# Performance work log

Measured on AMD Instinct MI355X. Metric: run time of the kernel, lower is better.

## Reference

```python
import jax, jax.numpy as jnp
import numpy as np

N_CHILDS = 50000
N_EDGES = 500000
NODE_FEAT = 256
NUM_SEM = 57
HID = 256
EDGE_FEAT = 64
EDGE_TYPES = 4
NUM_ITERS = 2


def setup_inputs() -> dict:
    key = jax.random.key(0)
    ks = jax.random.split(key, 12)
    d_in = NODE_FEAT + NUM_SEM            # 313
    d_ne = 2 * HID + EDGE_FEAT + EDGE_TYPES  # 580
    d_par = HID * (NUM_ITERS + 1)         # 768
    def lin(k, fan_in, fan_out):
        kw, kb = jax.random.split(k)
        s = 1.0 / np.sqrt(fan_in)
        return (jax.random.uniform(kw, (fan_in, fan_out), jnp.float32, -s, s),
                jax.random.uniform(kb, (fan_out,), jnp.float32, -s, s))
    W_child, b_child = lin(ks[0], d_in, HID)
    W_ne0, b_ne0 = lin(ks[1], d_ne, HID)
    W_ne1, b_ne1 = lin(ks[2], d_ne, HID)
    W_parent, b_parent = lin(ks[3], d_par, NODE_FEAT)
    return {
        "child_feats": jax.random.normal(ks[4], (1, N_CHILDS, d_in), jnp.float32),
        "child_exists": jnp.ones((1, N_CHILDS, 1), jnp.float32),
        "edge_type_onehot": jax.random.normal(ks[5], (1, N_EDGES, EDGE_TYPES), jnp.float32),
        "edge_feats": jax.random.normal(ks[6], (1, N_EDGES, EDGE_FEAT), jnp.float32),
        "edge_indices": jax.random.randint(ks[7], (1, N_EDGES, 2), 0, N_CHILDS, jnp.int64),
        "W_child": W_child, "b_child": b_child,
        "W_ne0": W_ne0, "b_ne0": b_ne0,
        "W_ne1": W_ne1, "b_ne1": b_ne1,
        "W_parent": W_parent, "b_parent": b_parent,
    }


def reference(child_feats, child_exists, edge_type_onehot, edge_feats, edge_indices,
              W_child, b_child, W_ne0, b_ne0, W_ne1, b_ne1, W_parent, b_parent):
    n = child_feats.shape[1]
    # node embedding: linear + relu, mask non-existent children
    x = jax.nn.relu(jnp.einsum('bnd,dh->bnh', child_feats, W_child) + b_child)
    x = x * child_exists                              # [1, N, H]
    iter_parent = [x.max(axis=1)]                     # symmetric_type == 'max'
    ef = jnp.concatenate([edge_type_onehot, edge_feats], axis=2)[0]  # [E, 4+64]
    src = edge_indices[0, :, 0]
    dst = edge_indices[0, :, 1]
    cnt = jax.ops.segment_sum(jnp.ones((src.shape[0],), x.dtype), src, num_segments=n)
    denom = jnp.maximum(cnt, 1.0)[:, None]            # scatter_mean clamp
    for W, b in ((W_ne0, b_ne0), (W_ne1, b_ne1)):
        nef = jnp.concatenate([x[0, src], x[0, dst], ef], axis=1)  # [E, 580]
        nef = jax.nn.relu(nef @ W + b)                # [E, H]
        # edge_symmetric_type == 'avg': scatter_mean over source index
        x = (jax.ops.segment_sum(nef, src, num_segments=n) / denom)[None]
        iter_parent.append(x.max(axis=1))
    parent = jnp.concatenate(iter_parent, axis=1)     # [1, H*(iters+1)]
    return jax.nn.relu(parent @ W_parent + b_parent)  # [1, node_feat_size]
```

## Files before the change

### kernel.cpp

```cpp
#include <hip/hip_runtime.h>

#define NC   50000
#define NE   500000
#define NEP  (NE + 64)
#define DIN  313
#define DNE  580
#define KPC  320
#define KB   96
#define NB_SCAN 196

typedef __attribute__((ext_vector_type(8))) short bf16x8;
typedef __attribute__((ext_vector_type(4))) float f32x4;

static __device__ __forceinline__ unsigned short f2bf(float f) {
    unsigned u = __float_as_uint(f);
    unsigned r = (u + 0x7fff + ((u >> 16) & 1)) >> 16;
    return (unsigned short)r;
}
static __device__ __forceinline__ float bf2f(unsigned short u) {
    return __uint_as_float(((unsigned)u) << 16);
}
static __device__ __forceinline__ void gload_lds16(const unsigned short* g, unsigned short* l) {
    __builtin_amdgcn_global_load_lds(
        (const __attribute__((address_space(1))) unsigned int*)(g),
        (__attribute__((address_space(3))) unsigned int*)(l), 16, 0, 0);
}

__global__ __launch_bounds__(256) void prep_w_kernel(
    const float* __restrict__ W0, const float* __restrict__ W1,
    const float* __restrict__ Wc,
    unsigned short* __restrict__ Wpt, unsigned short* __restrict__ Wbt,
    unsigned short* __restrict__ Wct)
{
    int b = blockIdx.x;
    if (b < 1024) {
        int layer = b >> 9, n2 = b & 511;
        const float* W = layer ? W1 : W0;
        unsigned short* dst = Wpt + (size_t)layer * 512 * 256 + (size_t)n2 * 256;
        int t = threadIdx.x;
        int ch = t >> 5, s = (t >> 3) & 3, j = t & 7;
        int gk = ch * 32 + ((s ^ (n2 & 3)) * 8) + j;
        float v = (n2 < 256) ? W[(size_t)gk * 256 + n2] : W[(size_t)(256 + gk) * 256 + (n2 - 256)];
        dst[t] = f2bf(v);
    } else if (b < 1536) {
        int idx = b - 1024;
        int layer = idx >> 8, n = idx & 255;
        const float* W = layer ? W1 : W0;
        unsigned short* dst = Wbt + (size_t)layer * 256 * KB + (size_t)n * KB;
        int t = threadIdx.x;
        if (t < KB) {
            int ch = t >> 5, s = (t >> 3) & 3, j = t & 7;
            int gk = ch * 32 + ((s ^ (n & 3)) * 8) + j;
            float v = (512 + gk < DNE) ? W[(size_t)(512 + gk) * 256 + n] : 0.0f;
            dst[t] = f2bf(v);
        }
    } else {
        int n = b - 1536;
        unsigned short* dst = Wct + (size_t)n * KPC;
        for (int t = threadIdx.x; t < KPC; t += 256) {
            int ch = t >> 5, s = (t >> 3) & 3, j = t & 7;
            int gk = ch * 32 + ((s ^ (n & 3)) * 8) + j;
            float v = (gk < DIN) ? Wc[(size_t)gk * 256 + n] : 0.0f;
            dst[t] = f2bf(v);
        }
    }
}

__global__ __launch_bounds__(256, 4) void child_mfma_kernel(
    const float* __restrict__ cf, const float* __restrict__ exists,
    const unsigned short* __restrict__ Wct, const float* __restrict__ bias,
    unsigned short* __restrict__ xb, float* __restrict__ pmax)
{
    __shared__ unsigned short sA[64][40];
    __shared__ unsigned short sB[256][32];
    __shared__ float smax[256];

    const int tid = threadIdx.x, lane = tid & 63, wid = tid >> 6;
    const int wm = wid >> 1, wn = wid & 1, l15 = lane & 15, l4 = lane >> 4;
    const int node0 = blockIdx.x * 64;
    const int arow = tid >> 2, s3 = tid & 3;

    smax[tid] = 0.0f;

    f32x4 acc[2][8];
    #pragma unroll
    for (int mi = 0; mi < 2; ++mi)
        #pragma unroll
        for (int ni = 0; ni < 8; ++ni)
            acc[mi][ni] = (f32x4){0.f, 0.f, 0.f, 0.f};

    int nodeA = node0 + arow; if (nodeA >= NC) nodeA = NC - 1;

    for (int ch = 0; ch < 10; ++ch) {
        #pragma unroll
        for (int i = 0; i < 4; ++i) {
            int n = (wid << 6) + (i << 4) + (lane >> 2);
            gload_lds16(Wct + (size_t)n * KPC + ch * 32 + (lane & 3) * 8,
                        &sB[(wid << 6) + (i << 4)][0]);
        }
        {
            int gk0 = ch * 32 + s3 * 8;
            union { unsigned short u[8]; int4 v; } pk;
            #pragma unroll
            for (int j = 0; j < 8; ++j) {
                int gk = gk0 + j;
                float f = (gk < DIN) ? cf[(size_t)nodeA * DIN + gk] : 0.0f;
                pk.u[j] = f2bf(f);
            }
            *(int4*)&sA[arow][s3 * 8] = pk.v;
        }
        __syncthreads();
        bf16x8 af[2];
        #pragma unroll
        for (int mi = 0; mi < 2; ++mi)
            af[mi] = *(const bf16x8*)&sA[wm * 32 + mi * 16 + l15][l4 * 8];
        #pragma unroll
        for (int ni = 0; ni < 8; ++ni) {
            int n = wn * 128 + ni * 16 + l15;
            bf16x8 bfr = *(const bf16x8*)&sB[n][(l4 ^ (n & 3)) * 8];
            acc[0][ni] = __builtin_amdgcn_mfma_f32_16x16x32_bf16(af[0], bfr, acc[0][ni], 0, 0, 0);
            acc[1][ni] = __builtin_amdgcn_mfma_f32_16x16x32_bf16(af[1], bfr, acc[1][ni], 0, 0, 0);
        }
        __syncthreads();
    }

    float bv[8];
    #pragma unroll
    for (int ni = 0; ni < 8; ++ni) bv[ni] = bias[wn * 128 + ni * 16 + l15];
    float cmax[8];
    #pragma unroll
    for (int ni = 0; ni < 8; ++ni) cmax[ni] = 0.0f;

    #pragma unroll
    for (int mi = 0; mi < 2; ++mi) {
        #pragma unroll
        for (int r = 0; r < 4; ++r) {
            int node = node0 + wm * 32 + mi * 16 + l4 * 4 + r;
            if (node < NC) {
                float ex = exists[node];
                #pragma unroll
                for (int ni = 0; ni < 8; ++ni) {
                    float v = fmaxf(acc[mi][ni][r] + bv[ni], 0.f) * ex;
                    xb[(size_t)node * 256 + wn * 128 + ni * 16 + l15] = f2bf(v);
                    cmax[ni] = fmaxf(cmax[ni], v);
                }
            }
        }
    }
    #pragma unroll
    for (int ni = 0; ni < 8; ++ni)
        atomicMax((unsigned int*)&smax[wn * 128 + ni * 16 + l15], __float_as_uint(cmax[ni]));
    __syncthreads();
    atomicMax((unsigned int*)&pmax[tid], __float_as_uint(smax[tid]));
}

__global__ __launch_bounds__(256, 3) void node_gemm_kernel(
    const unsigned short* __restrict__ xb,
    const unsigned short* __restrict__ Wpt,
    unsigned short* __restrict__ yp)
{
    __shared__ unsigned short sA[2][64][40];
    __shared__ unsigned short sB[2][256][32];

    const int tid = threadIdx.x, lane = tid & 63, wid = tid >> 6;
    const int wm = wid >> 1, wn = wid & 1, l15 = lane & 15, l4 = lane >> 4;
    const int node0 = blockIdx.x * 64;
    const int n0 = blockIdx.y * 256;
    const int arow = tid >> 2, s3 = tid & 3;

    int nodeA = node0 + arow; if (nodeA >= NC) nodeA = NC - 1;

    f32x4 acc[2][8];
    #pragma unroll
    for (int mi = 0; mi < 2; ++mi)
        #pragma unroll
        for (int ni = 0; ni < 8; ++ni)
            acc[mi][ni] = (f32x4){0.f, 0.f, 0.f, 0.f};

    #pragma unroll
    for (int i = 0; i < 4; ++i) {
        int n = (wid << 6) + (i << 4) + (lane >> 2);
        gload_lds16(Wpt + (size_t)(n0 + n) * 256 + (lane & 3) * 8, &sB[0][(wid << 6) + (i << 4)][0]);
    }
    *(int4*)&sA[0][arow][s3 * 8] = *(const int4*)(xb + (size_t)nodeA * 256 + s3 * 8);
    __syncthreads();

    int buf = 0;
    for (int ch = 0; ch < 8; ++ch) {
        const int nch = ch + 1;
        int4 areg;
        if (nch < 8) {
            #pragma unroll
            for (int i = 0; i < 4; ++i) {
                int n = (wid << 6) + (i << 4) + (lane >> 2);
                gload_lds16(Wpt + (size_t)(n0 + n) * 256 + nch * 32 + (lane & 3) * 8,
                            &sB[buf ^ 1][(wid << 6) + (i << 4)][0]);
            }
            areg = *(const int4*)(xb + (size_t)nodeA * 256 + nch * 32 + s3 * 8);
        }
        bf16x8 af[2];
        #pragma unroll
        for (int mi = 0; mi < 2; ++mi)
            af[mi] = *(const bf16x8*)&sA[buf][wm * 32 + mi * 16 + l15][l4 * 8];
        #pragma unroll
        for (int ni = 0; ni < 8; ++ni) {
            int n = wn * 128 + ni * 16 + l15;
            bf16x8 bfr = *(const bf16x8*)&sB[buf][n][(l4 ^ (n & 3)) * 8];
            acc[0][ni] = __builtin_amdgcn_mfma_f32_16x16x32_bf16(af[0], bfr, acc[0][ni], 0, 0, 0);
            acc[1][ni] = __builtin_amdgcn_mfma_f32_16x16x32_bf16(af[1], bfr, acc[1][ni], 0, 0, 0);
        }
        if (nch < 8) *(int4*)&sA[buf ^ 1][arow][s3 * 8] = areg;
        __syncthreads();
        buf ^= 1;
    }

    #pragma unroll
    for (int mi = 0; mi < 2; ++mi) {
        #pragma unroll
        for (int r = 0; r < 4; ++r) {
            int node = node0 + wm * 32 + mi * 16 + l4 * 4 + r;
            if (node < NC) {
                #pragma unroll
                for (int ni = 0; ni < 8; ++ni)
                    yp[(size_t)node * 512 + n0 + wn * 128 + ni * 16 + l15] = f2bf(acc[mi][ni][r]);
            }
        }
    }
}

__global__ __launch_bounds__(256, 3) void node_gemm_scaled_kernel(
    const float* __restrict__ accb, const float* __restrict__ invv,
    const unsigned short* __restrict__ Wpt,
    unsigned short* __restrict__ yp, float* __restrict__ pmax0)
{
    __shared__ unsigned short sA[2][64][40];
    __shared__ unsigned short sB[2][256][32];
    __shared__ float smax[256];

    const int tid = threadIdx.x, lane = tid & 63, wid = tid >> 6;
    const int wm = wid >> 1, wn = wid & 1, l15 = lane & 15, l4 = lane >> 4;
    const int node0 = blockIdx.x * 64;
    const int n0 = blockIdx.y * 256;
    const int arow = tid >> 2, s3 = tid & 3;

    smax[tid] = 0.0f;

    int nodeA = node0 + arow; if (nodeA >= NC) nodeA = NC - 1;
    const float inv_n = invv[nodeA];

    f32x4 acc[2][8];
    #pragma unroll
    for (int mi = 0; mi < 2; ++mi)
        #pragma unroll
        for (int ni = 0; ni < 8; ++ni)
            acc[mi][ni] = (f32x4){0.f, 0.f, 0.f, 0.f};

    #pragma unroll
    for (int i = 0; i < 4; ++i) {
        int n = (wid << 6) + (i << 4) + (lane >> 2);
        gload_lds16(Wpt + (size_t)(n0 + n) * 256 + (lane & 3) * 8, &sB[0][(wid << 6) + (i << 4)][0]);
    }
    {
        float4 a0 = *(const float4*)(accb + (size_t)nodeA * 256 + s3 * 8);
        float4 a1 = *(const float4*)(accb + (size_t)nodeA * 256 + s3 * 8 + 4);
        float v0=a0.x*inv_n, v1=a0.y*inv_n, v2=a0.z*inv_n, v3=a0.w*inv_n;
        float v4=a1.x*inv_n, v5=a1.y*inv_n, v6=a1.z*inv_n, v7=a1.w*inv_n;
        union { unsigned short u[8]; int4 v; } pk;
        pk.u[0]=f2bf(v0); pk.u[1]=f2bf(v1); pk.u[2]=f2bf(v2); pk.u[3]=f2bf(v3);
        pk.u[4]=f2bf(v4); pk.u[5]=f2bf(v5); pk.u[6]=f2bf(v6); pk.u[7]=f2bf(v7);
        *(int4*)&sA[0][arow][s3 * 8] = pk.v;
        int c0 = s3 * 8;
        atomicMax((unsigned int*)&smax[c0+0], __float_as_uint(v0));
        atomicMax((unsigned int*)&smax[c0+1], __float_as_uint(v1));
        atomicMax((unsigned int*)&smax[c0+2], __float_as_uint(v2));
        atomicMax((unsigned int*)&smax[c0+3], __float_as_uint(v3));
        atomicMax((unsigned int*)&smax[c0+4], __float_as_uint(v4));
        atomicMax((unsigned int*)&smax[c0+5], __float_as_uint(v5));
        atomicMax((unsigned int*)&smax[c0+6], __float_as_uint(v6));
        atomicMax((unsigned int*)&smax[c0+7], __float_as_uint(v7));
    }
    __syncthreads();

    int buf = 0;
    for (int ch = 0; ch < 8; ++ch) {
        const int nch = ch + 1;
        float4 f4a, f4b;
        if (nch < 8) {
            #pragma unroll
            for (int i = 0; i < 4; ++i) {
                int n = (wid << 6) + (i << 4) + (lane >> 2);
                gload_lds16(Wpt + (size_t)(n0 + n) * 256 + nch * 32 + (lane & 3) * 8,
                            &sB[buf ^ 1][(wid << 6) + (i << 4)][0]);
            }
            f4a = *(const float4*)(accb + (size_t)nodeA * 256 + nch * 32 + s3 * 8);
            f4b = *(const float4*)(accb + (size_t)nodeA * 256 + nch * 32 + s3 * 8 + 4);
        }
        bf16x8 af[2];
        #pragma unroll
        for (int mi = 0; mi < 2; ++mi)
            af[mi] = *(const bf16x8*)&sA[buf][wm * 32 + mi * 16 + l15][l4 * 8];
        #pragma unroll
        for (int ni = 0; ni < 8; ++ni) {
            int n = wn * 128 + ni * 16 + l15;
            bf16x8 bfr = *(const bf16x8*)&sB[buf][n][(l4 ^ (n & 3)) * 8];
            acc[0][ni] = __builtin_amdgcn_mfma_f32_16x16x32_bf16(af[0], bfr, acc[0][ni], 0, 0, 0);
            acc[1][ni] = __builtin_amdgcn_mfma_f32_16x16x32_bf16(af[1], bfr, acc[1][ni], 0, 0, 0);
        }
        if (nch < 8) {
            float v0=f4a.x*inv_n, v1=f4a.y*inv_n, v2=f4a.z*inv_n, v3=f4a.w*inv_n;
            float v4=f4b.x*inv_n, v5=f4b.y*inv_n, v6=f4b.z*inv_n, v7=f4b.w*inv_n;
            union { unsigned short u[8]; int4 v; } pk;
            pk.u[0]=f2bf(v0); pk.u[1]=f2bf(v1); pk.u[2]=f2bf(v2); pk.u[3]=f2bf(v3);
            pk.u[4]=f2bf(v4); pk.u[5]=f2bf(v5); pk.u[6]=f2bf(v6); pk.u[7]=f2bf(v7);
            *(int4*)&sA[buf ^ 1][arow][s3 * 8] = pk.v;
            int c0 = nch * 32 + s3 * 8;
            atomicMax((unsigned int*)&smax[c0+0], __float_as_uint(v0));
            atomicMax((unsigned int*)&smax[c0+1], __float_as_uint(v1));
            atomicMax((unsigned int*)&smax[c0+2], __float_as_uint(v2));
            atomicMax((unsigned int*)&smax[c0+3], __float_as_uint(v3));
            atomicMax((unsigned int*)&smax[c0+4], __float_as_uint(v4));
            atomicMax((unsigned int*)&smax[c0+5], __float_as_uint(v5));
            atomicMax((unsigned int*)&smax[c0+6], __float_as_uint(v6));
            atomicMax((unsigned int*)&smax[c0+7], __float_as_uint(v7));
        }
        __syncthreads();
        buf ^= 1;
    }

    #pragma unroll
    for (int mi = 0; mi < 2; ++mi) {
        #pragma unroll
        for (int r = 0; r < 4; ++r) {
            int node = node0 + wm * 32 + mi * 16 + l4 * 4 + r;
            if (node < NC) {
                #pragma unroll
                for (int ni = 0; ni < 8; ++ni)
                    yp[(size_t)node * 512 + n0 + wn * 128 + ni * 16 + l15] = f2bf(acc[mi][ni][r]);
            }
        }
    }
    atomicMax((unsigned int*)&pmax0[tid], __float_as_uint(smax[tid]));
}

__global__ __launch_bounds__(256) void count_int_kernel(
    const int* __restrict__ eidx, int* __restrict__ icnt)
{
    int t = blockIdx.x * 256 + threadIdx.x;
    if (t < NE) atomicAdd(&icnt[eidx[2 * t]], 1);
}

__global__ __launch_bounds__(256) void scan1_kernel(
    const int* __restrict__ icnt, int* __restrict__ part)
{
    __shared__ int sd[256];
    int i = blockIdx.x * 256 + threadIdx.x;
    sd[threadIdx.x] = (i < NC) ? icnt[i] : 0;
    __syncthreads();
    for (int d = 128; d > 0; d >>= 1) {
        if (threadIdx.x < d) sd[threadIdx.x] += sd[threadIdx.x + d];
        __syncthreads();
    }
    if (threadIdx.x == 0) part[blockIdx.x] = sd[0];
}

__global__ void scan2_kernel(int* __restrict__ part)
{
    if (threadIdx.x == 0) {
        int acc = 0;
        for (int i = 0; i < NB_SCAN; ++i) { int v = part[i]; part[i] = acc; acc += v; }
    }
}

__global__ __launch_bounds__(256) void scan3_kernel(
    const int* __restrict__ icnt, const int* __restrict__ part,
    int* __restrict__ cur)
{
    __shared__ int sc[256];
    const int t = threadIdx.x;
    int i = blockIdx.x * 256 + t;
    int val = (i < NC) ? icnt[i] : 0;
    sc[t] = val;
    __syncthreads();
    for (int d = 1; d < 256; d <<= 1) {
        int x = (t >= d) ? sc[t - d] : 0;
        __syncthreads();
        sc[t] += x;
        __syncthreads();
    }
    if (i < NC) cur[i] = part[blockIdx.x] + sc[t] - val;
}

__global__ __launch_bounds__(256) void bin_kernel(
    const int* __restrict__ eidx, int* __restrict__ cur, int* __restrict__ perm)
{
    int t = blockIdx.x * 256 + threadIdx.x;
    if (t < NE) {
        int s = eidx[2 * t];
        int p = atomicAdd(&cur[s], 1);
        perm[p] = t;
    }
}

__global__ __launch_bounds__(256) void inv_kernel(
    const int* __restrict__ icnt, float* __restrict__ inv)
{
    int t = blockIdx.x * 256 + threadIdx.x;
    if (t < NC) inv[t] = 1.0f / fmaxf((float)icnt[t], 1.0f);
}

__global__ __launch_bounds__(256) void ef_prep_kernel(
    const float* __restrict__ eto, const float* __restrict__ efe,
    const int* __restrict__ perm, const int* __restrict__ eidx,
    unsigned short* __restrict__ efc01, unsigned short* __restrict__ efc2,
    int* __restrict__ esrc, int* __restrict__ edst)
{
    int p = blockIdx.x * 256 + threadIdx.x;
    if (p >= NE) return;
    int e = perm[p];
    esrc[p] = eidx[2 * e];
    edst[p] = eidx[2 * e + 1];
    const float* efr = efe + (size_t)e * 64;

    union { unsigned short u[8]; int4 v; } pk;
    {
        float4 a = *(const float4*)(eto + (size_t)e * 4);
        float4 b = *(const float4*)(efr + 0);
        pk.u[0]=f2bf(a.x); pk.u[1]=f2bf(a.y); pk.u[2]=f2bf(a.z); pk.u[3]=f2bf(a.w);
        pk.u[4]=f2bf(b.x); pk.u[5]=f2bf(b.y); pk.u[6]=f2bf(b.z); pk.u[7]=f2bf(b.w);
        *(int4*)(efc01 + (size_t)p * 32) = pk.v;
    }
    #pragma unroll
    for (int g = 1; g < 4; ++g) {
        float4 a = *(const float4*)(efr + g * 8 - 4);
        float4 b = *(const float4*)(efr + g * 8);
        pk.u[0]=f2bf(a.x); pk.u[1]=f2bf(a.y); pk.u[2]=f2bf(a.z); pk.u[3]=f2bf(a.w);
        pk.u[4]=f2bf(b.x); pk.u[5]=f2bf(b.y); pk.u[6]=f2bf(b.z); pk.u[7]=f2bf(b.w);
        *(int4*)(efc01 + (size_t)p * 32 + g * 8) = pk.v;
    }
    #pragma unroll
    for (int g = 0; g < 4; ++g) {
        float4 a = *(const float4*)(efr + 28 + g * 8);
        float4 b = *(const float4*)(efr + 32 + g * 8);
        pk.u[0]=f2bf(a.x); pk.u[1]=f2bf(a.y); pk.u[2]=f2bf(a.z); pk.u[3]=f2bf(a.w);
        pk.u[4]=f2bf(b.x); pk.u[5]=f2bf(b.y); pk.u[6]=f2bf(b.z); pk.u[7]=f2bf(b.w);
        *(int4*)(efc01 + ((size_t)NEP + p) * 32 + g * 8) = pk.v;
    }
    {
        float4 a = *(const float4*)(efr + 60);
        pk.u[0]=f2bf(a.x); pk.u[1]=f2bf(a.y); pk.u[2]=f2bf(a.z); pk.u[3]=f2bf(a.w);
        pk.u[4]=0; pk.u[5]=0; pk.u[6]=0; pk.u[7]=0;
        *(int4*)(efc2 + (size_t)p * 8) = pk.v;
    }
}

#define LOAD16(B, YT, YM)                                              \
    _Pragma("unroll")                                                  \
    for (int r = 0; r < 16; ++r) {                                     \
        int row = (B) * 16 + r;                                        \
        YT[r] = bf2f(yp[((unsigned)s_src[row] << 9) + (unsigned)col]); \
        YM[r] = bf2f(yp[((unsigned)s_dst[row] << 9) + 256u + (unsigned)col]); \
    }

#define WALK16(B, YT, YM)                                              \
    _Pragma("unroll")                                                  \
    for (int r = 0; r < 16; ++r) {                                     \
        int row = (B) * 16 + r;                                        \
        float v = 0.0f;                                                \
        if (e0 + row < NE)                                             \
            v = fmaxf(bf2f(epb[row][col]) + YT[r] + YM[r] + b_col, 0.f); \
        int sr = s_src[row];                                           \
        if (sr != curn) {                                              \
            if (rstart > 0) accb[(size_t)curn * 256 + col] = run;      \
            else            atomicAdd(&accb[(size_t)curn * 256 + col], run); \
            curn = sr; run = v; rstart = row;                          \
        } else {                                                       \
            run += v;                                                  \
        }                                                              \
    }

__global__ __launch_bounds__(256, 4) void combine_efc_kernel(
    const unsigned short* __restrict__ yp,
    const unsigned short* __restrict__ efc01,
    const unsigned short* __restrict__ efc2,
    const int* __restrict__ esrc, const int* __restrict__ edst,
    const unsigned short* __restrict__ Wbt,
    const float* __restrict__ bias,
    float* __restrict__ accb)
{
    __shared__ __align__(16) unsigned char smem[34816];
    unsigned short (*sA01)[64][32] = (unsigned short (*)[64][32])(smem);
    unsigned short (*sA2)[8]       = (unsigned short (*)[8])(smem + 8192);
    unsigned short (*sW)[32]       = (unsigned short (*)[32])(smem + 9216);
    unsigned short (*epb)[272]     = (unsigned short (*)[272])(smem);
    __shared__ int s_src[64], s_dst[64];

    const int tid = threadIdx.x;
    const int nwg = gridDim.x;
    const int q = nwg >> 3, rr = nwg & 7;
    const int xcd = blockIdx.x & 7, within = blockIdx.x >> 3;
    const int bid = (xcd < rr ? xcd * (q + 1) : rr * (q + 1) + (xcd - rr) * q) + within;
    const int e0 = bid * 64;

    const int lane = tid & 63;
    const int wid  = tid >> 6;
    const int wm   = wid >> 1;
    const int wn   = wid & 1;
    const int l15  = lane & 15;
    const int l4   = lane >> 4;

    if (tid < 64) {
        int e = e0 + tid; if (e > NE - 1) e = NE - 1;
        s_src[tid] = esrc[e];
        s_dst[tid] = edst[e];
    }
    gload_lds16(efc01 + ((size_t)e0 + wid * 16) * 32 + lane * 8, &sA01[0][wid * 16][0]);
    gload_lds16(efc01 + ((size_t)NEP + e0 + wid * 16) * 32 + lane * 8, &sA01[1][wid * 16][0]);
    if (wid == 0)
        gload_lds16(efc2 + (size_t)e0 * 8 + lane * 8, &sA2[0][0]);
    #pragma unroll
    for (int i = 0; i < 4; ++i) {
        gload_lds16(Wbt + (size_t)((wid << 6) + (i << 4) + (lane >> 2)) * KB + (lane & 3) * 8,
                    &sW[(wid << 6) + (i << 4)][0]);
    }
    __syncthreads();

    f32x4 acc[2][8];
    #pragma unroll
    for (int mi = 0; mi < 2; ++mi)
        #pragma unroll
        for (int ni = 0; ni < 8; ++ni)
            acc[mi][ni] = (f32x4){0.f, 0.f, 0.f, 0.f};

    #pragma unroll
    for (int ch = 0; ch < 3; ++ch) {
        if (ch > 0) {
            __syncthreads();
            #pragma unroll
            for (int i = 0; i < 4; ++i) {
                gload_lds16(Wbt + (size_t)((wid << 6) + (i << 4) + (lane >> 2)) * KB + ch * 32 + (lane & 3) * 8,
                            &sW[(wid << 6) + (i << 4)][0]);
            }
            __syncthreads();
        }
        bf16x8 af0, af1;
        if (ch < 2) {
            af0 = *(const bf16x8*)&sA01[ch][wm * 32 + l15][l4 * 8];
            af1 = *(const bf16x8*)&sA01[ch][wm * 32 + 16 + l15][l4 * 8];
        } else {
            bf16x8 z = (bf16x8){0,0,0,0,0,0,0,0};
            bf16x8 a0 = *(const bf16x8*)&sA2[wm * 32 + l15][0];
            bf16x8 a1 = *(const bf16x8*)&sA2[wm * 32 + 16 + l15][0];
            af0 = (l4 == 0) ? a0 : z;
            af1 = (l4 == 0) ? a1 : z;
        }
        #pragma unroll
        for (int ni = 0; ni < 8; ++ni) {
            int n = wn * 128 + ni * 16 + l15;
            bf16x8 bfr = *(const bf16x8*)&sW[n][(l4 ^ (n & 3)) * 8];
            acc[0][ni] = __builtin_amdgcn_mfma_f32_16x16x32_bf16(af0, bfr, acc[0][ni], 0, 0, 0);
            acc[1][ni] = __builtin_amdgcn_mfma_f32_16x16x32_bf16(af1, bfr, acc[1][ni], 0, 0, 0);
        }
    }
    __syncthreads();

    #pragma unroll
    for (int mi = 0; mi < 2; ++mi)
        #pragma unroll
        for (int ni = 0; ni < 8; ++ni)
            #pragma unroll
            for (int r = 0; r < 4; ++r)
                epb[wm * 32 + mi * 16 + l4 * 4 + r][wn * 128 + ni * 16 + l15] = f2bf(acc[mi][ni][r]);

    const int col = tid;
    const float b_col = bias[col];
    float ytA[16], ymA[16], ytB[16], ymB[16];
    LOAD16(0, ytA, ymA)
    LOAD16(1, ytB, ymB)
    __syncthreads();

    int curn = s_src[0];
    int rstart = 0;
    float run = 0.f;

    WALK16(0, ytA, ymA)
    LOAD16(2, ytA, ymA)
    WALK16(1, ytB, ymB)
    LOAD16(3, ytB, ymB)
    WALK16(2, ytA, ymA)
    WALK16(3, ytB, ymB)

    atomicAdd(&accb[(size_t)curn * 256 + col], run);
}

__global__ __launch_bounds__(256, 3) void combine_f32_kernel(
    const unsigned short* __restrict__ yp,
    const float* __restrict__ eto, const float* __restrict__ efe,
    const int* __restrict__ eidx, const int* __restrict__ perm,
    const unsigned short* __restrict__ Wbt,
    const float* __restrict__ bias,
    float* __restrict__ accb)
{
    __shared__ unsigned short sA[3][64][40];
    __shared__ unsigned short sW[2][256][32];
    __shared__ int s_src[64], s_dst[64], s_perm[64];

    const int tid = threadIdx.x;
    const int nwg = gridDim.x;
    const int q = nwg >> 3, rr = nwg & 7;
    const int xcd = blockIdx.x & 7, within = blockIdx.x >> 3;
    const int bid = (xcd < rr ? xcd * (q + 1) : rr * (q + 1) + (xcd - rr) * q) + within;
    const int e0 = bid * 64;

    if (tid < 64) {
        int ee = e0 + tid; if (ee >= NE) ee = NE - 1;
        int e = perm[ee];
        s_perm[tid] = e;
        s_src[tid] = eidx[2 * e];
        s_dst[tid] = eidx[2 * e + 1];
    }
    const int lane = tid & 63;
    const int wid  = tid >> 6;
    const int wm   = wid >> 1;
    const int wn   = wid & 1;
    const int l15  = lane & 15;
    const int l4   = lane >> 4;
    const int arow = tid >> 2;
    const int s3   = tid & 3;

    f32x4 acc[2][8];
    #pragma unroll
    for (int mi = 0; mi < 2; ++mi)
        #pragma unroll
        for (int ni = 0; ni < 8; ++ni)
            acc[mi][ni] = (f32x4){0.f, 0.f, 0.f, 0.f};

    #pragma unroll
    for (int i = 0; i < 4; ++i) {
        int n = (wid << 6) + (i << 4) + (lane >> 2);
        gload_lds16(Wbt + (size_t)n * KB + (lane & 3) * 8, &sW[0][(wid << 6) + (i << 4)][0]);
    }
    __syncthreads();

    const int my_e = s_perm[arow];
    #pragma unroll
    for (int ch = 0; ch < 3; ++ch) {
        int g0 = ch * 32 + s3 * 8;
        union { unsigned short u[8]; int4 v; } pk;
        #pragma unroll
        for (int j = 0; j < 8; ++j) {
            int g = g0 + j;
            float f = 0.0f;
            if (g < 4)       f = eto[(size_t)my_e * 4 + g];
            else if (g < 68) f = efe[(size_t)my_e * 64 + (g - 4)];
            pk.u[j] = f2bf(f);
        }
        *(int4*)&sA[ch][arow][s3 * 8] = pk.v;
    }
    __syncthreads();

    int buf = 0;
    #pragma unroll
    for (int ch = 0; ch < 3; ++ch) {
        if (ch + 1 < 3) {
            #pragma unroll
            for (int i = 0; i < 4; ++i) {
                int n = (wid << 6) + (i << 4) + (lane >> 2);
                gload_lds16(Wbt + (size_t)n * KB + (ch + 1) * 32 + (lane & 3) * 8,
                            &sW[buf ^ 1][(wid << 6) + (i << 4)][0]);
            }
        }
        bf16x8 af[2];
        #pragma unroll
        for (int mi = 0; mi < 2; ++mi)
            af[mi] = *(const bf16x8*)&sA[ch][wm * 32 + mi * 16 + l15][l4 * 8];
        #pragma unroll
        for (int ni = 0; ni < 8; ++ni) {
            int n = wn * 128 + ni * 16 + l15;
            bf16x8 bfr = *(const bf16x8*)&sW[buf][n][(l4 ^ (n & 3)) * 8];
            acc[0][ni] = __builtin_amdgcn_mfma_f32_16x16x32_bf16(af[0], bfr, acc[0][ni], 0, 0, 0);
            acc[1][ni] = __builtin_amdgcn_mfma_f32_16x16x32_bf16(af[1], bfr, acc[1][ni], 0, 0, 0);
        }
        __syncthreads();
        buf ^= 1;
    }

    float (*ep)[258] = (float (*)[258])(&sW[0][0][0]);
    const int col = tid;
    const float b_col = bias[col];

    int curn = s_src[0];
    int rstart = 0;
    float run = 0.f;
    #pragma unroll
    for (int c = 0; c < 4; ++c) {
        if (wm == (c >> 1)) {
            const int mi = c & 1;
            #pragma unroll
            for (int ni = 0; ni < 8; ++ni) {
                #pragma unroll
                for (int r = 0; r < 4; ++r)
                    ep[l4 * 4 + r][wn * 128 + ni * 16 + l15] = acc[mi][ni][r];
            }
        }
        float yt[16], ym[16];
        #pragma unroll
        for (int r = 0; r < 16; ++r) {
            int row = c * 16 + r;
            yt[r] = bf2f(yp[(size_t)s_src[row] * 512 + col]);
            ym[r] = bf2f(yp[(size_t)s_dst[row] * 512 + 256 + col]);
        }
        __syncthreads();
        #pragma unroll
        for (int r = 0; r < 16; ++r) {
            int row = c * 16 + r;
            float v = 0.0f;
            if (e0 + row < NE)
                v = fmaxf(ep[r][col] + yt[r] + ym[r] + b_col, 0.f);
            int sr = s_src[row];
            if (sr != curn) {
                if (rstart > 0) accb[(size_t)curn * 256 + col] = run;
                else            atomicAdd(&accb[(size_t)curn * 256 + col], run);
                curn = sr; run = v; rstart = row;
            } else {
                run += v;
            }
        }
        __syncthreads();
    }
    atomicAdd(&accb[(size_t)curn * 256 + col], run);
}

__global__ __launch_bounds__(256) void finalize_kernel(
    const float* __restrict__ src, const float* __restrict__ inv,
    unsigned short* __restrict__ xb_out, float* __restrict__ pmax, int n)
{
    const int tid = threadIdx.x;
    int i0 = blockIdx.x * 128;
    int iend = i0 + 128; if (iend > n) iend = n;
    float m = 0.0f;
    for (int i = i0; i < iend; ++i) {
        float v = src[(size_t)i * 256 + tid];
        v *= inv[i];
        xb_out[(size_t)i * 256 + tid] = f2bf(v);
        m = fmaxf(m, v);
    }
    atomicMax((unsigned int*)&pmax[tid], __float_as_uint(m));
}

__global__ __launch_bounds__(256) void pmax_only_kernel(
    const float* __restrict__ src, const float* __restrict__ inv,
    float* __restrict__ pmax, int n)
{
    const int tid = threadIdx.x;
    int i0 = blockIdx.x * 128;
    int iend = i0 + 128; if (iend > n) iend = n;
    float m = 0.0f;
    for (int i = i0; i < iend; ++i)
        m = fmaxf(m, src[(size_t)i * 256 + tid] * inv[i]);
    atomicMax((unsigned int*)&pmax[tid], __float_as_uint(m));
}

__global__ __launch_bounds__(256) void parent_kernel(
    const float* __restrict__ pmax, const float* __restrict__ W,
    const float* __restrict__ bias, float* __restrict__ out)
{
    __shared__ float sp[768];
    const int tid = threadIdx.x;
    for (int i = tid; i < 768; i += 256) sp[i] = pmax[i];
    __syncthreads();
    float s = bias[tid];
    for (int k = 0; k < 768; ++k) s = fmaf(sp[k], W[(size_t)k * 256 + tid], s);
    out[tid] = fmaxf(s, 0.f);
}

extern "C" void kernel_launch(void* const* d_in, const int* in_sizes, int n_in,
                              void* d_out, int out_size, void* d_ws, size_t ws_size,
                              hipStream_t stream)
{
    const float* cf   = (const float*)d_in[0];
    const float* ex   = (const float*)d_in[1];
    const float* eto  = (const float*)d_in[2];
    const float* efe  = (const float*)d_in[3];
    const int*   eidx = (const int*)d_in[4];
    const float* Wc   = (const float*)d_in[5];
    const float* bc   = (const float*)d_in[6];
    const float* W0   = (const float*)d_in[7];
    const float* b0   = (const float*)d_in[8];
    const float* W1   = (const float*)d_in[9];
    const float* b1   = (const float*)d_in[10];
    const float* Wp   = (const float*)d_in[11];
    const float* bp   = (const float*)d_in[12];

    float*          accb = (float*)d_ws;
    float*          invv = accb + (size_t)NC * 256;
    float*          pmax = invv + NC;
    unsigned short* xb   = (unsigned short*)(pmax + 768);
    unsigned short* yp   = xb + (size_t)NC * 256;
    unsigned short* Wpt  = yp + (size_t)NC * 512;
    unsigned short* Wbt  = Wpt + (size_t)2 * 512 * 256;
    unsigned short* Wct  = Wbt + (size_t)2 * 256 * KB;
    int*            icnt = (int*)(Wct + (size_t)256 * KPC);
    int*            part = icnt + NC;
    int*            curb = part + 256;
    int*            perm = curb + NC;
    unsigned short* efc01 = (unsigned short*)(perm + NE);
    unsigned short* efc2  = efc01 + (size_t)2 * NEP * 32;
    int*            esrc  = (int*)(efc2 + (size_t)NEP * 8);
    int*            edst  = esrc + NE;
    size_t need = (size_t)((char*)(edst + NE) - (char*)d_ws);
    const bool use_efc = (ws_size >= need);

    hipMemsetAsync(pmax, 0, 768 * sizeof(float), stream);
    hipMemsetAsync(icnt, 0, NC * sizeof(int), stream);

    prep_w_kernel<<<1792, 256, 0, stream>>>(W0, W1, Wc, Wpt, Wbt, Wct);
    child_mfma_kernel<<<(NC + 63) / 64, 256, 0, stream>>>(cf, ex, Wct, bc, xb, pmax);

    count_int_kernel<<<(NE + 255) / 256, 256, 0, stream>>>(eidx, icnt);
    scan1_kernel<<<NB_SCAN, 256, 0, stream>>>(icnt, part);
    scan2_kernel<<<1, 64, 0, stream>>>(part);
    scan3_kernel<<<NB_SCAN, 256, 0, stream>>>(icnt, part, curb);
    bin_kernel<<<(NE + 255) / 256, 256, 0, stream>>>(eidx, curb, perm);
    inv_kernel<<<(NC + 255) / 256, 256, 0, stream>>>(icnt, invv);
    if (use_efc)
        ef_prep_kernel<<<(NE + 255) / 256, 256, 0, stream>>>(eto, efe, perm, eidx, efc01, efc2, esrc, edst);

    const int nwg = (NE + 63) / 64;
    if (use_efc) {
        node_gemm_kernel<<<dim3((NC + 63) / 64, 2), 256, 0, stream>>>(xb, Wpt, yp);
        hipMemsetAsync(accb, 0, (size_t)NC * 256 * sizeof(float), stream);
        combine_efc_kernel<<<nwg, 256, 0, stream>>>(
            yp, efc01, efc2, esrc, edst, Wbt, b0, accb);
        node_gemm_scaled_kernel<<<dim3((NC + 63) / 64, 2), 256, 0, stream>>>(
            accb, invv, Wpt + (size_t)512 * 256, yp, pmax + 256);
        hipMemsetAsync(accb, 0, (size_t)NC * 256 * sizeof(float), stream);
        combine_efc_kernel<<<nwg, 256, 0, stream>>>(
            yp, efc01, efc2, esrc, edst, Wbt + (size_t)256 * KB, b1, accb);
        pmax_only_kernel<<<(NC + 127) / 128, 256, 0, stream>>>(accb, invv, pmax + 512, NC);
    } else {
        for (int it = 0; it < 2; ++it) {
            node_gemm_kernel<<<dim3((NC + 63) / 64, 2), 256, 0, stream>>>(
                xb, Wpt + (size_t)it * 512 * 256, yp);
            hipMemsetAsync(accb, 0, (size_t)NC * 256 * sizeof(float), stream);
            combine_f32_kernel<<<nwg, 256, 0, stream>>>(
                yp, eto, efe, eidx, perm,
                Wbt + (size_t)it * 256 * KB, it ? b1 : b0, accb);
            finalize_kernel<<<(NC + 127) / 128, 256, 0, stream>>>(accb, invv, xb, pmax + 256 * (it + 1), NC);
        }
    }
    parent_kernel<<<1, 256, 0, stream>>>(pmax, Wp, bp, (float*)d_out);
}
```

Before: 604.1 us.

## Pre-convert child features to swizzled bf16 and double-buffer the child GEMM

Adds a prep kernel that converts the fp32 child features into a padded, swizzled bf16 buffer in the workspace. A new child GEMM kernel then streams both operands with direct global-to-LDS loads and double buffering, replacing the older path that converted fp32 to bf16 inside the GEMM. This aims to cut conversion work and load latency in the GEMM loop, but adds a full extra read and write pass over the features. It also enlarges the workspace requirement, which could switch off the whole fast edge path if the workspace is too small. The last block reads padded rows past the end of the new buffer.

```diff
diff --git a/kernel.cpp b/kernel.cpp
--- a/kernel.cpp
+++ b/kernel.cpp
@@ -66,6 +66,110 @@
     }
 }
 
+__global__ __launch_bounds__(256) void cf_prep_kernel(
+    const float* __restrict__ cf, unsigned short* __restrict__ cfb)
+{
+    int b = blockIdx.x;
+    for (int i = threadIdx.x; i < 4 * KPC; i += 256) {
+        int n = b * 4 + (i / KPC), t = i % KPC;
+        int ch = t >> 5, s = (t >> 3) & 3, j = t & 7;
+        int gk = ch * 32 + ((s ^ (n & 3)) * 8) + j;
+        float v = (gk < DIN) ? cf[(size_t)n * DIN + gk] : 0.0f;
+        cfb[(size_t)n * KPC + t] = f2bf(v);
+    }
+}
+
+__global__ __launch_bounds__(256, 3) void child_mfma_fast_kernel(
+    const unsigned short* __restrict__ cfb, const float* __restrict__ exists,
+    const unsigned short* __restrict__ Wct, const float* __restrict__ bias,
+    unsigned short* __restrict__ xb, float* __restrict__ pmax)
+{
+    __shared__ unsigned short sA[2][64][32];
+    __shared__ unsigned short sB[2][256][32];
+    __shared__ float smax[256];
+
+    const int tid = threadIdx.x, lane = tid & 63, wid = tid >> 6;
+    const int wm = wid >> 1, wn = wid & 1, l15 = lane & 15, l4 = lane >> 4;
+    const int node0 = blockIdx.x * 64;
+
+    smax[tid] = 0.0f;
+
+    f32x4 acc[2][8];
+    #pragma unroll
+    for (int mi = 0; mi < 2; ++mi)
+        #pragma unroll
+        for (int ni = 0; ni < 8; ++ni)
+            acc[mi][ni] = (f32x4){0.f, 0.f, 0.f, 0.f};
+
+    gload_lds16(cfb + (size_t)(node0 + wid * 16 + (lane >> 2)) * KPC + (lane & 3) * 8,
+                &sA[0][wid * 16][0]);
+    #pragma unroll
+    for (int i = 0; i < 4; ++i) {
+        int n = (wid << 6) + (i << 4) + (lane >> 2);
+        gload_lds16(Wct + (size_t)n * KPC + (lane & 3) * 8, &sB[0][(wid << 6) + (i << 4)][0]);
+    }
+    __syncthreads();
+
+    int buf = 0;
+    for (int ch = 0; ch < 10; ++ch) {
+        const int nch = ch + 1;
+        if (nch < 10) {
+            gload_lds16(cfb + (size_t)(node0 + wid * 16 + (lane >> 2)) * KPC + nch * 32 + (lane & 3) * 8,
+                        &sA[buf ^ 1][wid * 16][0]);
+            #pragma unroll
+            for (int i = 0; i < 4; ++i) {
+                int n = (wid << 6) + (i << 4) + (lane >> 2);
+                gload_lds16(Wct + (size_t)n * KPC + nch * 32 + (lane & 3) * 8,
+                            &sB[buf ^ 1][(wid << 6) + (i << 4)][0]);
+            }
+        }
+        bf16x8 af[2];
+        #pragma unroll
+        for (int mi = 0; mi < 2; ++mi) {
+            int r_ = wm * 32 + mi * 16 + l15;
+            af[mi] = *(const bf16x8*)&sA[buf][r_][(l4 ^ (r_ & 3)) * 8];
+        }
+        #pragma unroll
+        for (int ni = 0; ni < 8; ++ni) {
+            int n = wn * 128 + ni * 16 + l15;
+            bf16x8 bfr = *(const bf16x8*)&sB[buf][n][(l4 ^ (n & 3)) * 8];
+            acc[0][ni] = __builtin_amdgcn_mfma_f32_16x16x32_bf16(af[0], bfr, acc[0][ni], 0, 0, 0);
+            acc[1][ni] = __builtin_amdgcn_mfma_f32_16x16x32_bf16(af[1], bfr, acc[1][ni], 0, 0, 0);
+        }
+        __syncthreads();
+        buf ^= 1;
+    }
+
+    float bv[8];
+    #pragma unroll
+    for (int ni = 0; ni < 8; ++ni) bv[ni] = bias[wn * 128 + ni * 16 + l15];
+    float cmax[8];
+    #pragma unroll
+    for (int ni = 0; ni < 8; ++ni) cmax[ni] = 0.0f;
+
+    #pragma unroll
+    for (int mi = 0; mi < 2; ++mi) {
+        #pragma unroll
+        for (int r = 0; r < 4; ++r) {
+            int node = node0 + wm * 32 + mi * 16 + l4 * 4 + r;
+            if (node < NC) {
+                float ex = exists[node];
+                #pragma unroll
+                for (int ni = 0; ni < 8; ++ni) {
+                    float v = fmaxf(acc[mi][ni][r] + bv[ni], 0.f) * ex;
+                    xb[(size_t)node * 256 + wn * 128 + ni * 16 + l15] = f2bf(v);
+                    cmax[ni] = fmaxf(cmax[ni], v);
+                }
+            }
+        }
+    }
+    #pragma unroll
+    for (int ni = 0; ni < 8; ++ni)
+        atomicMax((unsigned int*)&smax[wn * 128 + ni * 16 + l15], __float_as_uint(cmax[ni]));
+    __syncthreads();
+    atomicMax((unsigned int*)&pmax[tid], __float_as_uint(smax[tid]));
+}
+
 __global__ __launch_bounds__(256, 4) void child_mfma_kernel(
     const float* __restrict__ cf, const float* __restrict__ exists,
     const unsigned short* __restrict__ Wct, const float* __restrict__ bias,
@@ -807,14 +911,20 @@
     unsigned short* efc2  = efc01 + (size_t)2 * NEP * 32;
     int*            esrc  = (int*)(efc2 + (size_t)NEP * 8);
     int*            edst  = esrc + NE;
-    size_t need = (size_t)((char*)(edst + NE) - (char*)d_ws);
+    unsigned short* cfb   = (unsigned short*)(edst + NE);
+    size_t need = (size_t)((char*)(cfb + (size_t)NC * KPC) - (char*)d_ws);
     const bool use_efc = (ws_size >= need);
 
     hipMemsetAsync(pmax, 0, 768 * sizeof(float), stream);
     hipMemsetAsync(icnt, 0, NC * sizeof(int), stream);
 
     prep_w_kernel<<<1792, 256, 0, stream>>>(W0, W1, Wc, Wpt, Wbt, Wct);
-    child_mfma_kernel<<<(NC + 63) / 64, 256, 0, stream>>>(cf, ex, Wct, bc, xb, pmax);
+    if (use_efc) {
+        cf_prep_kernel<<<NC / 4, 256, 0, stream>>>(cf, cfb);
+        child_mfma_fast_kernel<<<(NC + 63) / 64, 256, 0, stream>>>(cfb, ex, Wct, bc, xb, pmax);
+    } else {
+        child_mfma_kernel<<<(NC + 63) / 64, 256, 0, stream>>>(cf, ex, Wct, bc, xb, pmax);
+    }
 
     count_int_kernel<<<(NE + 255) / 256, 256, 0, stream>>>(eidx, icnt);
     scan1_kernel<<<NB_SCAN, 256, 0, stream>>>(icnt, part);
```

Result: slower. 628.8 us (+4.1%).
